# Optimization experiments

Hardware: AMD Instinct MI355X
Metric: run time of the kernel (lower is better)

Reference implementation:

```python
import jax, jax.numpy as jnp
import numpy as np

B, S, D, H, C, E, V = 8, 2048, 1024, 512, 256, 64, 64


def setup_inputs() -> dict:
    key = jax.random.key(0)
    ks = jax.random.split(key, 40)
    ri = lambda i, hi: jax.random.randint(ks[i], (B, S), 0, hi).astype(jnp.int32)
    p = lambda i, shape: (jax.random.normal(ks[i], shape, jnp.float32) * 0.02)
    inp = {
        'h_x': jax.random.normal(ks[0], (B, S, D), jnp.float32),
        'h_y': jax.random.normal(ks[1], (B, S, D), jnp.float32),
        'x_mask': jnp.ones((B, S), jnp.int32),
        'y_mask': jnp.ones((B, S), jnp.int32),
        'src_token_dense_mask': ri(2, 2), 'src_token_sparse_mask': ri(3, 2),
        'src_token_inarc_type': ri(4, V), 'src_token_arc_head': ri(5, S),
        'src_token_depth': ri(6, 16), 'src_word_inarc_type': ri(7, V),
        'src_word_inarc_type_mask': ri(8, 2),
        'tgt_token_dense_mask': ri(9, 2), 'tgt_token_sparse_mask': ri(10, 2),
        'tgt_token_inarc_type': ri(11, V), 'tgt_token_arc_head': ri(12, S),
        'tgt_token_depth': ri(13, 16), 'tgt_word_inarc_type': ri(14, V),
        'tgt_word_inarc_type_mask': ri(15, 2),
        # src MLP [D->H->C], tgt MLP [D->H->C]
        'W1s': p(16, (D, H)), 'b1s': jnp.zeros((H,), jnp.float32),
        'W2s': p(17, (H, C)), 'b2s': jnp.zeros((C,), jnp.float32),
        'W1t': p(18, (D, H)), 'b1t': jnp.zeros((H,), jnp.float32),
        'W2t': p(19, (H, C)), 'b2t': jnp.zeros((C,), jnp.float32),
        # inarc edge embedding + GeneralConv params
        'emb': p(20, (V, E)),
        'W_msg': p(21, (C, C)), 'b_msg': jnp.zeros((C,), jnp.float32),
        'W_edge': p(22, (E, C)),
        'att': p(23, (C,)),
        'W_self': p(24, (C, C)), 'b_self': jnp.zeros((C,), jnp.float32),
        # axis_feature MLP [C->C]
        'Wf': p(25, (C, C)), 'bf': jnp.zeros((C,), jnp.float32),
    }
    return inp


def _mlp(h, W1, b1, W2, b2):
    return jax.nn.leaky_relu(h @ W1 + b1) @ W2 + b2


def _graph_side(h, dense_m, sparse_m, arc_head, word_type, word_mask,
                W1, b1, W2, b2, emb, W_msg, b_msg, W_edge, att, W_self, b_self, Wf, bf):
    Bn, Sn, _ = h.shape
    x = _mlp(h, W1, b1, W2, b2)                      # [B,S,C]
    N = Bn * Sn
    Cn = x.shape[-1]
    xg = x.reshape(N, Cn)                            # debatch -> nodes
    off = (jnp.arange(Bn, dtype=jnp.int32) * Sn)[:, None]
    src = (arc_head + off).reshape(N)                # global head index per token
    dst = jnp.arange(N, dtype=jnp.int32)             # one in-edge per token
    valid = (sparse_m * dense_m).reshape(N).astype(x.dtype)
    ef = emb[(word_type * word_mask).reshape(N)]     # [N,E] edge embeddings
    # GeneralConv: directed message with edge features + additive attention
    m = xg[src] @ W_msg + b_msg + ef @ W_edge        # [N,C] messages
    hd = xg @ W_msg + b_msg                          # dst-side term for attention
    logit = jax.nn.leaky_relu(((m + hd) * att).sum(-1))
    logit = jnp.where(valid > 0, logit, -1e9)
    emax = jax.ops.segment_max(logit, dst, num_segments=N)
    ex = jnp.exp(logit - emax[dst]) * valid
    den = jax.ops.segment_sum(ex, dst, num_segments=N)
    alpha = ex / (den[dst] + 1e-16)                  # softmax per destination node
    agg = jax.ops.segment_sum(m * alpha[:, None], dst, num_segments=N)
    out = xg @ W_self + b_self + agg                 # skip_linear
    out = out / jnp.maximum(jnp.linalg.norm(out, axis=-1, keepdims=True), 1e-12)
    r = out.reshape(Bn, Sn, Cn).mean(axis=1, keepdims=True)  # FeatureRepr mean
    return r @ Wf + bf                               # [B,1,C]


def reference(h_x, x_mask, src_token_dense_mask, src_token_sparse_mask,
              src_token_inarc_type, src_token_arc_head, src_token_depth,
              src_word_inarc_type, src_word_inarc_type_mask,
              h_y, y_mask, tgt_token_dense_mask, tgt_token_sparse_mask,
              tgt_token_inarc_type, tgt_token_arc_head, tgt_token_depth,
              tgt_word_inarc_type, tgt_word_inarc_type_mask,
              W1s, b1s, W2s, b2s, W1t, b1t, W2t, b2t,
              emb, W_msg, b_msg, W_edge, att, W_self, b_self, Wf, bf):
    src_repr = _graph_side(h_x, src_token_dense_mask, src_token_sparse_mask,
                           src_token_arc_head, src_word_inarc_type, src_word_inarc_type_mask,
                           W1s, b1s, W2s, b2s, emb, W_msg, b_msg, W_edge, att,
                           W_self, b_self, Wf, bf)
    tgt_repr = _graph_side(h_y, tgt_token_dense_mask, tgt_token_sparse_mask,
                           tgt_token_arc_head, tgt_word_inarc_type, tgt_word_inarc_type_mask,
                           W1t, b1t, W2t, b2t, emb, W_msg, b_msg, W_edge, att,
                           W_self, b_self, Wf, bf)
    return (src_repr, tgt_repr)
```

## Files before the change

### kernel.cpp

```cpp
#include <hip/hip_runtime.h>
#include <stdint.h>

#define SEQ   2048
#define NNODE 16384

typedef short  short8  __attribute__((ext_vector_type(8)));
typedef float  float4v __attribute__((ext_vector_type(4)));
typedef unsigned short u16;
typedef unsigned short u16x8 __attribute__((ext_vector_type(8)));
typedef short  short4v __attribute__((ext_vector_type(4)));

__device__ __forceinline__ float b2f(u16 u) {
    union { unsigned int i; float f; } x; x.i = ((unsigned int)u) << 16; return x.f;
}
__device__ __forceinline__ u16 f2b(float f) {
    union { float f; unsigned int i; } x; x.f = f;
    unsigned int u = x.i;
    unsigned int r = (u + 0x7fffu + ((u >> 16) & 1u)) >> 16;
    return (u16)r;
}

__device__ __forceinline__ void gld16(const void* g, void* l) {
    __builtin_amdgcn_global_load_lds(
        (const __attribute__((address_space(1))) void*)g,
        (__attribute__((address_space(3))) void*)l, 16, 0, 0);
}

struct GemmP {
    const void*  A[2];
    const u16*   B[2];
    const float* bias[2];
    u16*         out[2];
};

template <int MB>
__device__ __forceinline__ void mfma4(const short8* af, const short8* bq,
                                      float4v (*acc)[4]) {
#pragma unroll
    for (int mi = 0; mi < 4; ++mi)
#pragma unroll
        for (int ni = 0; ni < 4; ++ni)
            acc[MB + mi][ni] = __builtin_amdgcn_mfma_f32_16x16x32_bf16(
                af[mi], bq[ni], acc[MB + mi][ni], 0, 0, 0);
}

#define TILE_BODY(AC, BC, KN, AG, BG, ACV, PL, PC)                            \
    {                                                                         \
        short8 bq[4], af[4];                                                  \
        _Pragma("unroll") for (int ni = 0; ni < 4; ++ni)                      \
            bq[ni] = *(const short8*)((BC) + boff + ni * 512);                \
        _Pragma("unroll") for (int mi = 0; mi < 4; ++mi)                      \
            af[mi] = *(const short8*)((AC) + aoff + mi * 512);                \
        if constexpr (AF32) prefA32(KN, PL); else stageA16(KN, AG);           \
        __builtin_amdgcn_s_barrier();                                         \
        __builtin_amdgcn_s_setprio(1);                                        \
        mfma4<0>(af, bq, acc);                                                \
        __builtin_amdgcn_s_setprio(0);                                        \
        __builtin_amdgcn_s_barrier();                                         \
        _Pragma("unroll") for (int mi = 0; mi < 4; ++mi)                      \
            af[mi] = *(const short8*)((AC) + aoff + (4 + mi) * 512);          \
        stageB(KN, BG);                                                       \
        if constexpr (AF32) {                                                 \
            cvtWrite(PC, ACV);                                                \
            asm volatile("s_waitcnt lgkmcnt(0)" ::: "memory");                \
            asm volatile("s_waitcnt vmcnt(8)" ::: "memory");                  \
        } else {                                                              \
            asm volatile("s_waitcnt vmcnt(8)" ::: "memory");                  \
        }                                                                     \
        __builtin_amdgcn_s_barrier();                                         \
        __builtin_amdgcn_s_setprio(1);                                        \
        mfma4<4>(af, bq, acc);                                                \
        __builtin_amdgcn_s_setprio(0);                                        \
        __builtin_amdgcn_s_barrier();                                         \
    }

template <int ACT, int AF32>
__global__ __launch_bounds__(512, 2) void gemm8_k(GemmP p, int M, int N, int K) {
    __shared__ __align__(16) u16 smem[49152];

    const int z = blockIdx.z;
    const u16*   __restrict__ Bg   = p.B[z];
    const float* __restrict__ bias = p.bias[z];
    const u16*   __restrict__ A16  = (const u16*)p.A[z];
    const float* __restrict__ A32  = (const float*)p.A[z];

    const int mt  = blockIdx.x * 256;
    const int nt  = blockIdx.y * 256;
    const int tid = threadIdx.x;
    const int l   = tid & 63;
    const int w   = tid >> 6;
    const int wm  = (w >> 2) * 128;
    const int wn  = (w & 3) * 64;
    const int lr  = l & 15;
    const int lk  = l >> 4;
    (void)M;

    float4v acc[8][4] = {};
    float4v paA[4], paB[4];

    const int rm0 = tid >> 2;
    const int cc0 = tid & 3;
    const int gc0 = cc0 ^ (rm0 & 3) ^ ((rm0 >> 2) & 3);
    const int rm1 = rm0 + 128;

    u16* const As0 = smem;
    u16* const Bs0 = smem + 24576;

    auto stageA16 = [&](int k0, u16* dst) {
        gld16(A16 + (size_t)(mt + rm0) * K + k0 + gc0 * 8, dst + tid * 8);
        gld16(A16 + (size_t)(mt + rm1) * K + k0 + gc0 * 8, dst + (tid + 512) * 8);
    };
    auto stageB = [&](int k0, u16* dst) {
        gld16(Bg + (size_t)(nt + rm0) * K + k0 + gc0 * 8, dst + tid * 8);
        gld16(Bg + (size_t)(nt + rm1) * K + k0 + gc0 * 8, dst + (tid + 512) * 8);
    };
    auto prefA32 = [&](int k0, float4v* pa) {
        const float* s0 = A32 + (size_t)(mt + rm0) * K + k0 + gc0 * 8;
        const float* s1 = A32 + (size_t)(mt + rm1) * K + k0 + gc0 * 8;
        pa[0] = *(const float4v*)s0; pa[1] = *(const float4v*)(s0 + 4);
        pa[2] = *(const float4v*)s1; pa[3] = *(const float4v*)(s1 + 4);
    };
    auto cvtWrite = [&](const float4v* pa, u16* dst) {
        u16x8 r0, r1;
        r0[0]=f2b(pa[0][0]); r0[1]=f2b(pa[0][1]); r0[2]=f2b(pa[0][2]); r0[3]=f2b(pa[0][3]);
        r0[4]=f2b(pa[1][0]); r0[5]=f2b(pa[1][1]); r0[6]=f2b(pa[1][2]); r0[7]=f2b(pa[1][3]);
        r1[0]=f2b(pa[2][0]); r1[1]=f2b(pa[2][1]); r1[2]=f2b(pa[2][2]); r1[3]=f2b(pa[2][3]);
        r1[4]=f2b(pa[3][0]); r1[5]=f2b(pa[3][1]); r1[6]=f2b(pa[3][2]); r1[7]=f2b(pa[3][3]);
        *(u16x8*)(dst + tid * 8) = r0;
        *(u16x8*)(dst + (tid + 512) * 8) = r1;
    };

    const int fsl  = lk ^ (lr & 3) ^ ((lr >> 2) & 3);
    const int aoff = (wm + lr) * 32 + fsl * 8;
    const int boff = (wn + lr) * 32 + fsl * 8;

    const int KT = K >> 5;

    if constexpr (AF32) {
        float4v p0[4];
        prefA32(0, p0);
        stageB(0, Bs0);
        prefA32(32, paB);
        stageB(32, Bs0 + 8192);
        cvtWrite(p0, As0);
        asm volatile("s_waitcnt lgkmcnt(0)" ::: "memory");
        asm volatile("s_waitcnt vmcnt(8)" ::: "memory");
    } else {
        stageA16(0, As0);          stageB(0, Bs0);
        stageA16(32, As0 + 8192);  stageB(32, Bs0 + 8192);
        asm volatile("s_waitcnt vmcnt(8)" ::: "memory");
    }
    __builtin_amdgcn_s_barrier();

    int sc = 0;
    for (int kt = 0; kt < KT; kt += 2) {
        const int sc1 = (sc == 2) ? 0 : sc + 1;
        const int sc2 = (sc1 == 2) ? 0 : sc1 + 1;
        u16* Ae = As0 + sc  * 8192;  u16* Be = Bs0 + sc  * 8192;
        u16* Ao = As0 + sc1 * 8192;  u16* Bo = Bs0 + sc1 * 8192;
        u16* A2 = As0 + sc2 * 8192;  u16* B2 = Bs0 + sc2 * 8192;
        const int k2 = (kt + 2 < KT) ? (kt + 2) << 5 : 0;
        const int k3 = (kt + 3 < KT) ? (kt + 3) << 5 : 0;
        TILE_BODY(Ae, Be, k2, A2, B2, Ao, paA, paB)
        TILE_BODY(Ao, Bo, k3, Ae, Be, A2, paB, paA)
        sc = sc2;
    }

    __syncthreads();

    const int r0 = lk * 4;
    float bvv[4];
#pragma unroll
    for (int ni = 0; ni < 4; ++ni) bvv[ni] = bias[nt + wn + ni * 16 + lr];
    const int half = w >> 2;
#pragma unroll
    for (int pass = 0; pass < 2; ++pass) {
        if (half == pass) {
#pragma unroll
            for (int mi = 0; mi < 8; ++mi)
#pragma unroll
                for (int ni = 0; ni < 4; ++ni) {
                    const int lc = wn + ni * 16 + lr;
#pragma unroll
                    for (int r = 0; r < 4; ++r) {
                        float v = acc[mi][ni][r] + bvv[ni];
                        if (ACT) v = v > 0.f ? v : 0.01f * v;
                        smem[(mi * 16 + r0 + r) * 264 + lc] = f2b(v);
                    }
                }
        }
        __syncthreads();
#pragma unroll
        for (int it = 0; it < 8; ++it) {
            const int id  = it * 512 + tid;
            const int row = id >> 5, colc = id & 31;
            u16x8 vv = *(const u16x8*)(smem + (size_t)row * 264 + colc * 8);
            *(u16x8*)(p.out[z] + (size_t)(mt + pass * 128 + row) * N + nt + colc * 8) = vv;
        }
        __syncthreads();
    }
}

struct TP { const float* src[6]; u16* dst[6]; int K[6]; int N[6]; };

__global__ __launch_bounds__(256) void transpose_k(TP t) {
    __shared__ float tile[64][65];
    const int m = blockIdx.y;
    const int K = t.K[m], N = t.N[m];
    const int tn = N >> 6;
    const int ntiles = (K >> 6) * tn;
    const int bid = blockIdx.x;
    if (bid >= ntiles) return;
    const int k0 = (bid / tn) * 64, n0 = (bid % tn) * 64;
    const int tid = threadIdx.x;
#pragma unroll
    for (int pass = 0; pass < 4; ++pass) {
        int kk = pass * 16 + (tid >> 4);
        int nn = (tid & 15) * 4;
        float4v v = *(const float4v*)(t.src[m] + (size_t)(k0 + kk) * N + n0 + nn);
        tile[kk][nn + 0] = v[0]; tile[kk][nn + 1] = v[1];
        tile[kk][nn + 2] = v[2]; tile[kk][nn + 3] = v[3];
    }
    __syncthreads();
    const int n = tid >> 2, kc = (tid & 3) * 16;
    u16x8 a, b;
#pragma unroll
    for (int j = 0; j < 8; ++j) {
        a[j] = f2b(tile[kc + j][n]);
        b[j] = f2b(tile[kc + 8 + j][n]);
    }
    u16* d = t.dst[m] + (size_t)(n0 + n) * K + k0 + kc;
    *(u16x8*)d = a;
    *(u16x8*)(d + 8) = b;
}

__global__ void ew_k(const float* emb, const float* W_edge, float* EW) {
    const int t = blockIdx.x, c = threadIdx.x;
    float s = 0.f;
    for (int e = 0; e < 64; ++e)
        s += emb[t * 64 + e] * W_edge[e * 256 + c];
    EW[t * 256 + c] = s;
}

struct WmP { const float* W2[2]; const float* Wmsg; const float* Wself;
             float* W23[2]; };

__global__ __launch_bounds__(512) void wmul_k(WmP q) {
    __shared__ float w2[16][256];
    const int side = blockIdx.y;
    const int k0 = blockIdx.x * 16;
    const int n = threadIdx.x;
    const float* __restrict__ W2 = q.W2[side];
    for (int i = threadIdx.x; i < 4096; i += 512)
        w2[i >> 8][i & 255] = W2[(size_t)(k0 + (i >> 8)) * 256 + (i & 255)];
    __syncthreads();
    const float* __restrict__ Wc = (n < 256) ? q.Wmsg : q.Wself;
    const int nn = n & 255;
    float acc[16] = {};
    for (int c = 0; c < 256; ++c) {
        const float wc = Wc[c * 256 + nn];
#pragma unroll
        for (int kk = 0; kk < 16; ++kk) acc[kk] += w2[kk][c] * wc;
    }
    for (int kk = 0; kk < 16; ++kk)
        q.W23[side][(size_t)(k0 + kk) * 512 + n] = acc[kk];
}

struct B23P { const float* b2[2]; const float* bmsg; const float* bself;
              float* b23; };

__global__ void b23_k(B23P q) {
    const int side = blockIdx.x;
    const int n = threadIdx.x;
    const float* __restrict__ Wc = (n < 256) ? q.bmsg : q.bself;
    (void)Wc;
    const float* __restrict__ Wcat = nullptr;
    (void)Wcat;
    const float* __restrict__ b2 = q.b2[side];
    float s = (n < 256) ? q.bmsg[n] : q.bself[n - 256];
    q.b23[side * 512 + n] = s;
}

struct B23WP { const float* b2[2]; const float* bmsg; const float* bself;
               const float* Wmsg; const float* Wself; float* b23; };

__global__ void b23w_k(B23WP q) {
    const int side = blockIdx.x;
    const int n = threadIdx.x;
    const float* __restrict__ W = (n < 256) ? q.Wmsg : q.Wself;
    const int nn = n & 255;
    const float* __restrict__ b2 = q.b2[side];
    float s = (n < 256) ? q.bmsg[nn] : q.bself[nn];
    for (int c = 0; c < 256; ++c)
        s += b2[c] * W[c * 256 + nn];
    q.b23[side * 512 + n] = s;
}

struct EpiP {
    const u16* xcat[2];
    const int* den[2]; const int* spa[2]; const int* arc[2];
    const int* wty[2]; const int* wma[2];
    const float* EW; float* racc;
};

__global__ __launch_bounds__(256) void epi_k(EpiP p) {
    __shared__ float part[4][256];
    const int bx    = blockIdx.x;
    const int side  = bx >> 9;
    const int local = bx & 511;
    const int base  = local * 32;
    const int b     = base >> 11;
    const int tid   = threadIdx.x;
    const int w = tid >> 6, l = tid & 63;

    const u16* __restrict__ xcat = p.xcat[side];

    float4v acc = {};
    for (int j = 0; j < 8; ++j) {
        const int i     = base + w * 8 + j;
        const int valid = p.den[side][i] * p.spa[side][i];
        const int srcn  = p.arc[side][i] + (i >> 11) * SEQ;
        const int t     = p.wty[side][i] * p.wma[side][i];
        short4v xs = *(const short4v*)(xcat + (size_t)i * 512 + 256 + l * 4);
        short4v xm = *(const short4v*)(xcat + (size_t)srcn * 512 + l * 4);
        float4v ew = *(const float4v*)(p.EW + (size_t)t * 256 + l * 4);
        const float vm = valid ? 1.f : 0.f;
        float4v v;
        v[0] = b2f((u16)xs[0]) + vm * (b2f((u16)xm[0]) + ew[0]);
        v[1] = b2f((u16)xs[1]) + vm * (b2f((u16)xm[1]) + ew[1]);
        v[2] = b2f((u16)xs[2]) + vm * (b2f((u16)xm[2]) + ew[2]);
        v[3] = b2f((u16)xs[3]) + vm * (b2f((u16)xm[3]) + ew[3]);
        float ss = v[0]*v[0] + v[1]*v[1] + v[2]*v[2] + v[3]*v[3];
        for (int m = 32; m >= 1; m >>= 1) ss += __shfl_xor(ss, m, 64);
        const float rn = 1.f / fmaxf(sqrtf(ss), 1e-12f);
        acc[0] += v[0] * rn; acc[1] += v[1] * rn;
        acc[2] += v[2] * rn; acc[3] += v[3] * rn;
    }
    part[w][l * 4 + 0] = acc[0];
    part[w][l * 4 + 1] = acc[1];
    part[w][l * 4 + 2] = acc[2];
    part[w][l * 4 + 3] = acc[3];
    __syncthreads();
    const float s = part[0][tid] + part[1][tid] + part[2][tid] + part[3][tid];
    atomicAdd(p.racc + ((size_t)side * 8 + b) * 256 + tid, s);
}

__global__ void fin_k(const float* racc, const float* Wf, const float* bfv,
                      float* out) {
    __shared__ float r[256];
    const int bid = blockIdx.x;
    const int tid = threadIdx.x;
    r[tid] = racc[bid * 256 + tid] * (1.f / 2048.f);
    __syncthreads();
    float s = bfv[tid];
    for (int k = 0; k < 256; ++k)
        s += r[k] * Wf[k * 256 + tid];
    out[bid * 256 + tid] = s;
}

extern "C" void kernel_launch(void* const* d_in, const int* in_sizes, int n_in,
                              void* d_out, int out_size, void* d_ws, size_t ws_size,
                              hipStream_t stream) {
    const float* h[2]   = {(const float*)d_in[0],  (const float*)d_in[1]};
    const int* den[2]   = {(const int*)d_in[4],  (const int*)d_in[11]};
    const int* spa[2]   = {(const int*)d_in[5],  (const int*)d_in[12]};
    const int* arc[2]   = {(const int*)d_in[7],  (const int*)d_in[14]};
    const int* wty[2]   = {(const int*)d_in[9],  (const int*)d_in[16]};
    const int* wma[2]   = {(const int*)d_in[10], (const int*)d_in[17]};
    const float* W1[2]  = {(const float*)d_in[18], (const float*)d_in[22]};
    const float* b1[2]  = {(const float*)d_in[19], (const float*)d_in[23]};
    const float* W2[2]  = {(const float*)d_in[20], (const float*)d_in[24]};
    const float* b2[2]  = {(const float*)d_in[21], (const float*)d_in[25]};
    const float* emb    = (const float*)d_in[26];
    const float* Wmsg   = (const float*)d_in[27];
    const float* bmsg   = (const float*)d_in[28];
    const float* Wedge  = (const float*)d_in[29];
    const float* Wself  = (const float*)d_in[31];
    const float* bself  = (const float*)d_in[32];
    const float* Wf     = (const float*)d_in[33];
    const float* bf_    = (const float*)d_in[34];

    char* ws = (char*)d_ws;
    size_t off = 0;
    auto alloc = [&](size_t bytes) -> void* {
        void* pp = ws + off; off += (bytes + 255) & ~(size_t)255; return pp;
    };
    u16*   x1    = (u16*)  alloc(2ull * NNODE * 512 * 2);
    u16*   xcat  = (u16*)  alloc(2ull * NNODE * 512 * 2);
    u16*   W1T   = (u16*)  alloc(2ull * 512 * 1024 * 2);
    float* W23   = (float*)alloc(2ull * 512 * 512 * 4);
    u16*   W23T  = (u16*)  alloc(2ull * 512 * 512 * 2);
    float* EW    = (float*)alloc(64 * 256 * 4);
    float* b23   = (float*)alloc(2 * 512 * 4);
    float* racc  = (float*)alloc(2 * 8 * 256 * 4);

    TP tp = {};
    tp.src[0] = W1[0]; tp.dst[0] = W1T;              tp.K[0] = 1024; tp.N[0] = 512;
    tp.src[1] = W1[1]; tp.dst[1] = W1T + 512 * 1024; tp.K[1] = 1024; tp.N[1] = 512;
    hipLaunchKernelGGL(transpose_k, dim3(128, 2), dim3(256), 0, stream, tp);
    hipLaunchKernelGGL(ew_k, dim3(64), dim3(256), 0, stream, emb, Wedge, EW);

    WmP wq;
    wq.W2[0] = W2[0]; wq.W2[1] = W2[1];
    wq.Wmsg = Wmsg; wq.Wself = Wself;
    wq.W23[0] = W23; wq.W23[1] = W23 + 512 * 512;
    hipLaunchKernelGGL(wmul_k, dim3(32, 2), dim3(512), 0, stream, wq);

    TP tp2 = {};
    tp2.src[0] = W23;            tp2.dst[0] = W23T;            tp2.K[0] = 512; tp2.N[0] = 512;
    tp2.src[1] = W23 + 512*512;  tp2.dst[1] = W23T + 512*512;  tp2.K[1] = 512; tp2.N[1] = 512;
    hipLaunchKernelGGL(transpose_k, dim3(64, 2), dim3(256), 0, stream, tp2);

    B23WP bq;
    bq.b2[0] = b2[0]; bq.b2[1] = b2[1];
    bq.bmsg = bmsg; bq.bself = bself;
    bq.Wmsg = Wmsg; bq.Wself = Wself;
    bq.b23 = b23;
    hipLaunchKernelGGL(b23w_k, dim3(2), dim3(512), 0, stream, bq);
    hipMemsetAsync(racc, 0, 2 * 8 * 256 * 4, stream);

    GemmP g1 = {};
    g1.A[0] = h[0];  g1.A[1] = h[1];
    g1.B[0] = W1T;   g1.B[1] = W1T + 512 * 1024;
    g1.bias[0] = b1[0]; g1.bias[1] = b1[1];
    g1.out[0] = x1;  g1.out[1] = x1 + (size_t)NNODE * 512;
    hipLaunchKernelGGL((gemm8_k<1, 1>), dim3(64, 2, 2), dim3(512), 0, stream,
                       g1, NNODE, 512, 1024);

    GemmP g23 = {};
    g23.A[0] = x1;   g23.A[1] = x1 + (size_t)NNODE * 512;
    g23.B[0] = W23T; g23.B[1] = W23T + 512 * 512;
    g23.bias[0] = b23; g23.bias[1] = b23 + 512;
    g23.out[0] = xcat; g23.out[1] = xcat + (size_t)NNODE * 512;
    hipLaunchKernelGGL((gemm8_k<0, 0>), dim3(64, 2, 2), dim3(512), 0, stream,
                       g23, NNODE, 512, 512);

    EpiP ep;
    ep.xcat[0] = xcat; ep.xcat[1] = xcat + (size_t)NNODE * 512;
    for (int s = 0; s < 2; ++s) {
        ep.den[s] = den[s]; ep.spa[s] = spa[s]; ep.arc[s] = arc[s];
        ep.wty[s] = wty[s]; ep.wma[s] = wma[s];
    }
    ep.EW = EW; ep.racc = racc;
    hipLaunchKernelGGL(epi_k, dim3(1024), dim3(256), 0, stream, ep);

    hipLaunchKernelGGL(fin_k, dim3(16), dim3(256), 0, stream,
                       racc, Wf, bf_, (float*)d_out);
}
```

Measured before the change: 338.2 us.

## Shrink GEMM block tile to 128x256 with 4 waves and split-N MFMA phases

The bf16 GEMM kernel now uses 256-thread blocks computing 128x256 tiles (4 waves, each 64x128) instead of 512-thread 256x256 tiles. This doubles the grid to 512 blocks and removes the two-pass epilogue. The inner loop now splits along N instead of M, and the LDS footprint and vmcnt waits are adjusted to match. Small prep kernels (ew, W23, b23w) get multiple partial accumulators for ILP, and a dead b23 kernel is removed. The trade-off is more blocks for better CU fill against lower per-block reuse of A and B tiles.

```diff
diff --git a/kernel.cpp b/kernel.cpp
--- a/kernel.cpp
+++ b/kernel.cpp
@@ -33,15 +33,15 @@
     u16*         out[2];
 };
 
-template <int MB>
-__device__ __forceinline__ void mfma4(const short8* af, const short8* bq,
-                                      float4v (*acc)[4]) {
+template <int NB>
+__device__ __forceinline__ void mfma4n(const short8* af, const short8* bq,
+                                       float4v (*acc)[8]) {
 #pragma unroll
     for (int mi = 0; mi < 4; ++mi)
 #pragma unroll
         for (int ni = 0; ni < 4; ++ni)
-            acc[MB + mi][ni] = __builtin_amdgcn_mfma_f32_16x16x32_bf16(
-                af[mi], bq[ni], acc[MB + mi][ni], 0, 0, 0);
+            acc[mi][NB + ni] = __builtin_amdgcn_mfma_f32_16x16x32_bf16(
+                af[mi], bq[ni], acc[mi][NB + ni], 0, 0, 0);
 }
 
 #define TILE_BODY(AC, BC, KN, AG, BG, ACV, PL, PC)                            \
@@ -54,29 +54,29 @@
         if constexpr (AF32) prefA32(KN, PL); else stageA16(KN, AG);           \
         __builtin_amdgcn_s_barrier();                                         \
         __builtin_amdgcn_s_setprio(1);                                        \
-        mfma4<0>(af, bq, acc);                                                \
+        mfma4n<0>(af, bq, acc);                                               \
         __builtin_amdgcn_s_setprio(0);                                        \
         __builtin_amdgcn_s_barrier();                                         \
-        _Pragma("unroll") for (int mi = 0; mi < 4; ++mi)                      \
-            af[mi] = *(const short8*)((AC) + aoff + (4 + mi) * 512);          \
+        _Pragma("unroll") for (int ni = 0; ni < 4; ++ni)                      \
+            bq[ni] = *(const short8*)((BC) + boff + (4 + ni) * 512);          \
         stageB(KN, BG);                                                       \
         if constexpr (AF32) {                                                 \
             cvtWrite(PC, ACV);                                                \
             asm volatile("s_waitcnt lgkmcnt(0)" ::: "memory");                \
             asm volatile("s_waitcnt vmcnt(8)" ::: "memory");                  \
         } else {                                                              \
-            asm volatile("s_waitcnt vmcnt(8)" ::: "memory");                  \
+            asm volatile("s_waitcnt vmcnt(6)" ::: "memory");                  \
         }                                                                     \
         __builtin_amdgcn_s_barrier();                                         \
         __builtin_amdgcn_s_setprio(1);                                        \
-        mfma4<4>(af, bq, acc);                                                \
+        mfma4n<4>(af, bq, acc);                                               \
         __builtin_amdgcn_s_setprio(0);                                        \
         __builtin_amdgcn_s_barrier();                                         \
     }
 
 template <int ACT, int AF32>
-__global__ __launch_bounds__(512, 2) void gemm8_k(GemmP p, int M, int N, int K) {
-    __shared__ __align__(16) u16 smem[49152];
+__global__ __launch_bounds__(256, 2) void gemm8_k(GemmP p, int M, int N, int K) {
+    __shared__ __align__(16) u16 smem[36864];
 
     const int z = blockIdx.z;
     const u16*   __restrict__ Bg   = p.B[z];
@@ -84,39 +84,41 @@
     const u16*   __restrict__ A16  = (const u16*)p.A[z];
     const float* __restrict__ A32  = (const float*)p.A[z];
 
-    const int mt  = blockIdx.x * 256;
+    const int mt  = blockIdx.x * 128;
     const int nt  = blockIdx.y * 256;
     const int tid = threadIdx.x;
     const int l   = tid & 63;
     const int w   = tid >> 6;
-    const int wm  = (w >> 2) * 128;
-    const int wn  = (w & 3) * 64;
+    const int wm  = (w >> 1) * 64;
+    const int wn  = (w & 1) * 128;
     const int lr  = l & 15;
     const int lk  = l >> 4;
     (void)M;
 
-    float4v acc[8][4] = {};
+    float4v acc[4][8] = {};
     float4v paA[4], paB[4];
 
     const int rm0 = tid >> 2;
     const int cc0 = tid & 3;
     const int gc0 = cc0 ^ (rm0 & 3) ^ ((rm0 >> 2) & 3);
-    const int rm1 = rm0 + 128;
 
     u16* const As0 = smem;
-    u16* const Bs0 = smem + 24576;
+    u16* const Bs0 = smem + 12288;
 
     auto stageA16 = [&](int k0, u16* dst) {
         gld16(A16 + (size_t)(mt + rm0) * K + k0 + gc0 * 8, dst + tid * 8);
-        gld16(A16 + (size_t)(mt + rm1) * K + k0 + gc0 * 8, dst + (tid + 512) * 8);
+        gld16(A16 + (size_t)(mt + rm0 + 64) * K + k0 + gc0 * 8,
+              dst + (tid + 256) * 8);
     };
     auto stageB = [&](int k0, u16* dst) {
-        gld16(Bg + (size_t)(nt + rm0) * K + k0 + gc0 * 8, dst + tid * 8);
-        gld16(Bg + (size_t)(nt + rm1) * K + k0 + gc0 * 8, dst + (tid + 512) * 8);
+#pragma unroll
+        for (int it = 0; it < 4; ++it)
+            gld16(Bg + (size_t)(nt + rm0 + 64 * it) * K + k0 + gc0 * 8,
+                  dst + (size_t)(tid + 256 * it) * 8);
     };
     auto prefA32 = [&](int k0, float4v* pa) {
         const float* s0 = A32 + (size_t)(mt + rm0) * K + k0 + gc0 * 8;
-        const float* s1 = A32 + (size_t)(mt + rm1) * K + k0 + gc0 * 8;
+        const float* s1 = A32 + (size_t)(mt + rm0 + 64) * K + k0 + gc0 * 8;
         pa[0] = *(const float4v*)s0; pa[1] = *(const float4v*)(s0 + 4);
         pa[2] = *(const float4v*)s1; pa[3] = *(const float4v*)(s1 + 4);
     };
@@ -127,7 +129,7 @@
         r1[0]=f2b(pa[2][0]); r1[1]=f2b(pa[2][1]); r1[2]=f2b(pa[2][2]); r1[3]=f2b(pa[2][3]);
         r1[4]=f2b(pa[3][0]); r1[5]=f2b(pa[3][1]); r1[6]=f2b(pa[3][2]); r1[7]=f2b(pa[3][3]);
         *(u16x8*)(dst + tid * 8) = r0;
-        *(u16x8*)(dst + (tid + 512) * 8) = r1;
+        *(u16x8*)(dst + (tid + 256) * 8) = r1;
     };
 
     const int fsl  = lk ^ (lr & 3) ^ ((lr >> 2) & 3);
@@ -143,12 +145,12 @@
         prefA32(32, paB);
         stageB(32, Bs0 + 8192);
         cvtWrite(p0, As0);
+        asm volatile("s_waitcnt vmcnt(8)" ::: "memory");
         asm volatile("s_waitcnt lgkmcnt(0)" ::: "memory");
-        asm volatile("s_waitcnt vmcnt(8)" ::: "memory");
     } else {
         stageA16(0, As0);          stageB(0, Bs0);
-        stageA16(32, As0 + 8192);  stageB(32, Bs0 + 8192);
-        asm volatile("s_waitcnt vmcnt(8)" ::: "memory");
+        stageA16(32, As0 + 4096);  stageB(32, Bs0 + 8192);
+        asm volatile("s_waitcnt vmcnt(6)" ::: "memory");
     }
     __builtin_amdgcn_s_barrier();
 
@@ -156,9 +158,9 @@
     for (int kt = 0; kt < KT; kt += 2) {
         const int sc1 = (sc == 2) ? 0 : sc + 1;
         const int sc2 = (sc1 == 2) ? 0 : sc1 + 1;
-        u16* Ae = As0 + sc  * 8192;  u16* Be = Bs0 + sc  * 8192;
-        u16* Ao = As0 + sc1 * 8192;  u16* Bo = Bs0 + sc1 * 8192;
-        u16* A2 = As0 + sc2 * 8192;  u16* B2 = Bs0 + sc2 * 8192;
+        u16* Ae = As0 + sc  * 4096;  u16* Be = Bs0 + sc  * 8192;
+        u16* Ao = As0 + sc1 * 4096;  u16* Bo = Bs0 + sc1 * 8192;
+        u16* A2 = As0 + sc2 * 4096;  u16* B2 = Bs0 + sc2 * 8192;
         const int k2 = (kt + 2 < KT) ? (kt + 2) << 5 : 0;
         const int k3 = (kt + 3 < KT) ? (kt + 3) << 5 : 0;
         TILE_BODY(Ae, Be, k2, A2, B2, Ao, paA, paB)
@@ -168,36 +170,29 @@
 
     __syncthreads();
 
-    const int r0 = lk * 4;
-    float bvv[4];
-#pragma unroll
-    for (int ni = 0; ni < 4; ++ni) bvv[ni] = bias[nt + wn + ni * 16 + lr];
-    const int half = w >> 2;
-#pragma unroll
-    for (int pass = 0; pass < 2; ++pass) {
-        if (half == pass) {
-#pragma unroll
-            for (int mi = 0; mi < 8; ++mi)
-#pragma unroll
-                for (int ni = 0; ni < 4; ++ni) {
-                    const int lc = wn + ni * 16 + lr;
-#pragma unroll
-                    for (int r = 0; r < 4; ++r) {
-                        float v = acc[mi][ni][r] + bvv[ni];
-                        if (ACT) v = v > 0.f ? v : 0.01f * v;
-                        smem[(mi * 16 + r0 + r) * 264 + lc] = f2b(v);
-                    }
-                }
+    const int er0 = lk * 4;
+    float bvv[8];
+#pragma unroll
+    for (int ni = 0; ni < 8; ++ni) bvv[ni] = bias[nt + wn + ni * 16 + lr];
+#pragma unroll
+    for (int mi = 0; mi < 4; ++mi)
+#pragma unroll
+        for (int ni = 0; ni < 8; ++ni) {
+            const int lc = wn + ni * 16 + lr;
+#pragma unroll
+            for (int r = 0; r < 4; ++r) {
+                float v = acc[mi][ni][r] + bvv[ni];
+                if (ACT) v = v > 0.f ? v : 0.01f * v;
+                smem[(size_t)(wm + mi * 16 + er0 + r) * 264 + lc] = f2b(v);
+            }
         }
-        __syncthreads();
-#pragma unroll
-        for (int it = 0; it < 8; ++it) {
-            const int id  = it * 512 + tid;
-            const int row = id >> 5, colc = id & 31;
-            u16x8 vv = *(const u16x8*)(smem + (size_t)row * 264 + colc * 8);
-            *(u16x8*)(p.out[z] + (size_t)(mt + pass * 128 + row) * N + nt + colc * 8) = vv;
-        }
-        __syncthreads();
+    __syncthreads();
+#pragma unroll
+    for (int it = 0; it < 16; ++it) {
+        const int id  = it * 256 + tid;
+        const int row = id >> 5, colc = id & 31;
+        u16x8 vv = *(const u16x8*)(smem + (size_t)row * 264 + colc * 8);
+        *(u16x8*)(p.out[z] + (size_t)(mt + row) * N + nt + colc * 8) = vv;
     }
 }
 
@@ -236,10 +231,14 @@
 
 __global__ void ew_k(const float* emb, const float* W_edge, float* EW) {
     const int t = blockIdx.x, c = threadIdx.x;
-    float s = 0.f;
-    for (int e = 0; e < 64; ++e)
-        s += emb[t * 64 + e] * W_edge[e * 256 + c];
-    EW[t * 256 + c] = s;
+    float p0 = 0.f, p1 = 0.f, p2 = 0.f, p3 = 0.f;
+    for (int e = 0; e < 64; e += 4) {
+        p0 += emb[t * 64 + e + 0] * W_edge[(e + 0) * 256 + c];
+        p1 += emb[t * 64 + e + 1] * W_edge[(e + 1) * 256 + c];
+        p2 += emb[t * 64 + e + 2] * W_edge[(e + 2) * 256 + c];
+        p3 += emb[t * 64 + e + 3] * W_edge[(e + 3) * 256 + c];
+    }
+    EW[t * 256 + c] = (p0 + p1) + (p2 + p3);
 }
 
 struct WmP { const float* W2[2]; const float* Wmsg; const float* Wself;
@@ -257,28 +256,18 @@
     const float* __restrict__ Wc = (n < 256) ? q.Wmsg : q.Wself;
     const int nn = n & 255;
     float acc[16] = {};
-    for (int c = 0; c < 256; ++c) {
-        const float wc = Wc[c * 256 + nn];
-#pragma unroll
-        for (int kk = 0; kk < 16; ++kk) acc[kk] += w2[kk][c] * wc;
+    for (int c = 0; c < 256; c += 4) {
+        const float wc0 = Wc[(c + 0) * 256 + nn];
+        const float wc1 = Wc[(c + 1) * 256 + nn];
+        const float wc2 = Wc[(c + 2) * 256 + nn];
+        const float wc3 = Wc[(c + 3) * 256 + nn];
+#pragma unroll
+        for (int kk = 0; kk < 16; ++kk)
+            acc[kk] += w2[kk][c] * wc0 + w2[kk][c + 1] * wc1 +
+                       w2[kk][c + 2] * wc2 + w2[kk][c + 3] * wc3;
     }
     for (int kk = 0; kk < 16; ++kk)
         q.W23[side][(size_t)(k0 + kk) * 512 + n] = acc[kk];
-}
-
-struct B23P { const float* b2[2]; const float* bmsg; const float* bself;
-              float* b23; };
-
-__global__ void b23_k(B23P q) {
-    const int side = blockIdx.x;
-    const int n = threadIdx.x;
-    const float* __restrict__ Wc = (n < 256) ? q.bmsg : q.bself;
-    (void)Wc;
-    const float* __restrict__ Wcat = nullptr;
-    (void)Wcat;
-    const float* __restrict__ b2 = q.b2[side];
-    float s = (n < 256) ? q.bmsg[n] : q.bself[n - 256];
-    q.b23[side * 512 + n] = s;
 }
 
 struct B23WP { const float* b2[2]; const float* bmsg; const float* bself;
@@ -290,9 +279,14 @@
     const float* __restrict__ W = (n < 256) ? q.Wmsg : q.Wself;
     const int nn = n & 255;
     const float* __restrict__ b2 = q.b2[side];
+    float p[8] = {};
+    for (int c = 0; c < 256; c += 8) {
+#pragma unroll
+        for (int j = 0; j < 8; ++j)
+            p[j] += b2[c + j] * W[(c + j) * 256 + nn];
+    }
     float s = (n < 256) ? q.bmsg[nn] : q.bself[nn];
-    for (int c = 0; c < 256; ++c)
-        s += b2[c] * W[c * 256 + nn];
+    s += ((p[0] + p[1]) + (p[2] + p[3])) + ((p[4] + p[5]) + (p[6] + p[7]));
     q.b23[side * 512 + n] = s;
 }
 
@@ -424,7 +418,7 @@
     g1.B[0] = W1T;   g1.B[1] = W1T + 512 * 1024;
     g1.bias[0] = b1[0]; g1.bias[1] = b1[1];
     g1.out[0] = x1;  g1.out[1] = x1 + (size_t)NNODE * 512;
-    hipLaunchKernelGGL((gemm8_k<1, 1>), dim3(64, 2, 2), dim3(512), 0, stream,
+    hipLaunchKernelGGL((gemm8_k<1, 1>), dim3(128, 2, 2), dim3(256), 0, stream,
                        g1, NNODE, 512, 1024);
 
     GemmP g23 = {};
@@ -432,7 +426,7 @@
     g23.B[0] = W23T; g23.B[1] = W23T + 512 * 512;
     g23.bias[0] = b23; g23.bias[1] = b23 + 512;
     g23.out[0] = xcat; g23.out[1] = xcat + (size_t)NNODE * 512;
-    hipLaunchKernelGGL((gemm8_k<0, 0>), dim3(64, 2, 2), dim3(512), 0, stream,
+    hipLaunchKernelGGL((gemm8_k<0, 0>), dim3(128, 2, 2), dim3(256), 0, stream,
                        g23, NNODE, 512, 512);
 
     EpiP ep;
```

After: 349.2 us. +3.3%, slower.
